# Optimization experiments

Measured on AMD Instinct MI355X. Metric: run time of the kernel, lower is better.

Reference implementation:

```python
import jax, jax.numpy as jnp
import numpy as np

B, S, D, E, H = 4, 2048, 1024, 8, 4096

def setup_inputs() -> dict:
    key = jax.random.key(0)
    ks = jax.random.split(key, 7)
    scale_d = 1.0 / np.sqrt(D)
    scale_h = 1.0 / np.sqrt(H)
    return {
        "x": jax.random.normal(ks[0], (B, S, D), dtype=jnp.float32),
        "Wr": jax.random.uniform(ks[1], (D, E), jnp.float32, -scale_d, scale_d),
        "br": jnp.zeros((E,), jnp.float32),
        "W1": jax.random.uniform(ks[2], (E, D, H), jnp.float32, -scale_d, scale_d),
        "b1": jax.random.uniform(ks[3], (E, H), jnp.float32, -scale_d, scale_d),
        "W2": jax.random.uniform(ks[4], (E, H, D), jnp.float32, -scale_h, scale_h),
        "b2": jax.random.uniform(ks[5], (E, D), jnp.float32, -scale_h, scale_h),
    }

def reference(x, Wr, br, W1, b1, W2, b2):
    # Router: softmax then argmax (top-1). Note: original does NOT scale
    # expert output by the routing weight and never applies capacity drop.
    route_logits = jnp.einsum("bsd,de->bse", x, Wr) + br
    routing_weights = jax.nn.softmax(route_logits, axis=-1)
    selected_expert = jnp.argmax(routing_weights, axis=-1)  # [B, S] int

    num_experts = W1.shape[0]
    out = jnp.zeros_like(x)
    # Fixed small loop over experts (structurally distinct weight slices);
    # select-by-mask keeps shapes static under jit.
    for e in range(num_experts):
        h = jax.nn.gelu(jnp.einsum("bsd,dh->bsh", x, W1[e]) + b1[e], approximate=False)
        y = jnp.einsum("bsh,hd->bsd", h, W2[e]) + b2[e]
        out = jnp.where((selected_expert == e)[..., None], y, out)
    return out
```

## Files before the change

kernel.cpp:

```cpp
#include <hip/hip_runtime.h>
#include <math.h>

#define TOK   8192
#define DD    1024
#define EE    8
#define HH    4096
#define MAXROWS 10240
#define MAXMT 40

typedef unsigned short u16;
typedef unsigned int   u32;
typedef __bf16 bf16x8 __attribute__((ext_vector_type(8)));
typedef float  f32x4  __attribute__((ext_vector_type(4)));

__device__ __forceinline__ u16 f2bf(float f) {
  union { float f; u32 u; } v; v.f = f;
  u32 r = v.u + 0x7fffu + ((v.u >> 16) & 1u);
  return (u16)(r >> 16);
}

__device__ __forceinline__ void gload16(const void* g, void* l) {
  __builtin_amdgcn_global_load_lds(
      (const __attribute__((address_space(1))) void*)g,
      (__attribute__((address_space(3))) void*)l, 16, 0, 0);
}

__global__ void k_init(int* rowmap, int* counts, int* fill) {
  int i = blockIdx.x * 256 + threadIdx.x;
  if (i < MAXROWS) rowmap[i] = -1;
  if (blockIdx.x == 0 && threadIdx.x < EE) { counts[threadIdx.x] = 0; fill[threadIdx.x] = 0; }
}

__global__ __launch_bounds__(256)
void k_route(const float* __restrict__ x, const float* __restrict__ Wr,
             const float* __restrict__ br, int* __restrict__ eid,
             int* __restrict__ counts, u16* __restrict__ xb) {
  int t = blockIdx.x * 4 + (threadIdx.x >> 6);
  int lt = threadIdx.x & 63;
  const float4* xr = (const float4*)(x + (size_t)t * DD);
  u16* xbr = xb + (size_t)t * DD;
  const float4* wrp = (const float4*)Wr;
  float acc[EE];
  #pragma unroll
  for (int e = 0; e < EE; ++e) acc[e] = 0.f;
  #pragma unroll
  for (int i = 0; i < 4; ++i) {
    int d4 = lt + 64 * i;
    float4 v = xr[d4];
    u32 p0 = (u32)f2bf(v.x) | ((u32)f2bf(v.y) << 16);
    u32 p1 = (u32)f2bf(v.z) | ((u32)f2bf(v.w) << 16);
    ((uint2*)xbr)[d4] = make_uint2(p0, p1);
    float vv[4] = { v.x, v.y, v.z, v.w };
    #pragma unroll
    for (int dd = 0; dd < 4; ++dd) {
      float xv = vv[dd];
      float4 a = wrp[(size_t)(d4 * 4 + dd) * 2];
      float4 b = wrp[(size_t)(d4 * 4 + dd) * 2 + 1];
      acc[0] += xv * a.x; acc[1] += xv * a.y; acc[2] += xv * a.z; acc[3] += xv * a.w;
      acc[4] += xv * b.x; acc[5] += xv * b.y; acc[6] += xv * b.z; acc[7] += xv * b.w;
    }
  }
  #pragma unroll
  for (int e = 0; e < EE; ++e)
    #pragma unroll
    for (int off = 32; off > 0; off >>= 1) acc[e] += __shfl_down(acc[e], off);
  if (lt == 0) {
    float best = -1e30f; int be = 0;
    #pragma unroll
    for (int e = 0; e < EE; ++e) {
      float v = acc[e] + br[e];
      if (v > best) { best = v; be = e; }
    }
    eid[t] = be;
    atomicAdd(&counts[be], 1);
  }
}

__global__ void k_scan(const int* __restrict__ counts, int* __restrict__ poff) {
  if (threadIdx.x == 0) {
    int off = 0; poff[0] = 0;
    for (int e = 0; e < EE; ++e) { off += ((counts[e] + 255) >> 8) << 8; poff[e + 1] = off; }
  }
}

__global__ void k_fillmap(const int* __restrict__ eid, const int* __restrict__ poff,
                          int* __restrict__ fill, int* __restrict__ rowmap) {
  int t = blockIdx.x * 256 + threadIdx.x;
  if (t < TOK) {
    int e = eid[t];
    int pos = atomicAdd(&fill[e], 1);
    rowmap[poff[e] + pos] = t;
  }
}

__global__ __launch_bounds__(256)
void k_transpose(const float* __restrict__ W, u16* __restrict__ WT, int K, int N) {
  __shared__ float tile[64][33];
  const int e = blockIdx.z;
  const int n0 = blockIdx.x * 32, k0 = blockIdx.y * 64;
  const float* We = W + (size_t)e * K * N;
  u16* WTe = WT + (size_t)e * K * N;
  const int t = threadIdx.x;
  const int kk = t >> 3, nn = (t & 7) * 4;
  #pragma unroll
  for (int i = 0; i < 2; ++i) {
    const float4 v = *(const float4*)&We[(size_t)(k0 + kk + 32 * i) * N + n0 + nn];
    tile[kk + 32 * i][nn]     = v.x;
    tile[kk + 32 * i][nn + 1] = v.y;
    tile[kk + 32 * i][nn + 2] = v.z;
    tile[kk + 32 * i][nn + 3] = v.w;
  }
  __syncthreads();
  const int n = t >> 3, c = t & 7;
  u32 p[4];
  #pragma unroll
  for (int j = 0; j < 4; ++j) {
    u32 lo = f2bf(tile[c * 8 + 2 * j][n]);
    u32 hi = f2bf(tile[c * 8 + 2 * j + 1][n]);
    p[j] = lo | (hi << 16);
  }
  *(uint4*)&WTe[(size_t)(n0 + n) * K + k0 + c * 8] = make_uint4(p[0], p[1], p[2], p[3]);
}

template <int KDIM, int NDIM, bool G2>
__global__ __launch_bounds__(512, 2)
void k_gemm(const u16* __restrict__ Abase, const u16* __restrict__ WT,
            const float* __restrict__ bias, const int* __restrict__ poff,
            const int* __restrict__ rowmap, u16* __restrict__ hout,
            float* __restrict__ yout) {
  extern __shared__ char lds[];
  const int mt = blockIdx.y;
  const int mbase = mt * 256;
  if (mbase >= poff[EE]) return;
  int e = 0;
  #pragma unroll
  for (int q = 1; q < EE; ++q) e += (mbase >= poff[q]) ? 1 : 0;

  const int nbase = blockIdx.x * 256;
  const int tid = threadIdx.x;
  const int lt = tid & 63;
  const int wid = tid >> 6;
  const int wr = wid >> 2, wc = wid & 3;

  const int row0 = tid >> 2;
  const int cl = (tid & 3) ^ ((tid >> 3) & 3);
  int r0, r1;
  if (G2) { r0 = mbase + row0; r1 = r0 + 128; }
  else {
    r0 = rowmap[mbase + row0];       if (r0 < 0) r0 = 0;
    r1 = rowmap[mbase + 128 + row0]; if (r1 < 0) r1 = 0;
  }
  const u16* gA0 = Abase + (size_t)r0 * KDIM + cl * 8;
  const u16* gA1 = Abase + (size_t)r1 * KDIM + cl * 8;
  const u16* wte = WT + (size_t)e * NDIM * KDIM + (size_t)nbase * KDIM;
  const u16* gB0 = wte + (size_t)row0 * KDIM + cl * 8;
  const u16* gB1 = wte + (size_t)(128 + row0) * KDIM + cl * 8;

  char* dA = lds + tid * 16;
  char* dB = lds + 65536 + tid * 16;

#define STAGE(B, T) do {                               \
    const int ko = (T) * 32;                           \
    gload16(gA0 + ko, dA + (B) * 16384);               \
    gload16(gA1 + ko, dA + (B) * 16384 + 8192);        \
    gload16(gB0 + ko, dB + (B) * 16384);               \
    gload16(gB1 + ko, dB + (B) * 16384 + 8192);        \
  } while (0)

  const int cph = ((lt >> 4) ^ ((lt >> 1) & 3)) << 4;
  const char* pA = lds + (wr * 128 + (lt & 15)) * 64 + cph;
  const char* pB = lds + 65536 + (wc * 64 + (lt & 15)) * 64 + cph;

  f32x4 acc[8][4] = {};

#define GSTEP(T, B, WAITI, DOSTAGE) do {                                              \
    asm volatile("s_waitcnt vmcnt(" WAITI ")\n\ts_barrier" ::: "memory");             \
    if (DOSTAGE) STAGE(((B) + 3) & 3, (T) + 3);                                       \
    bf16x8 af[8], bg[4];                                                              \
    _Pragma("unroll")                                                                 \
    for (int m = 0; m < 8; ++m) af[m] = *(const bf16x8*)(pA + (B) * 16384 + m * 1024);\
    _Pragma("unroll")                                                                 \
    for (int n = 0; n < 4; ++n) bg[n] = *(const bf16x8*)(pB + (B) * 16384 + n * 1024);\
    __builtin_amdgcn_s_setprio(1);                                                    \
    _Pragma("unroll")                                                                 \
    for (int m = 0; m < 8; ++m)                                                       \
      _Pragma("unroll")                                                               \
      for (int n = 0; n < 4; ++n)                                                     \
        acc[m][n] = __builtin_amdgcn_mfma_f32_16x16x32_bf16(af[m], bg[n], acc[m][n], 0, 0, 0); \
    __builtin_amdgcn_s_setprio(0);                                                    \
  } while (0)

  STAGE(0, 0); STAGE(1, 1); STAGE(2, 2);
  const int KT = KDIM / 32;
  #pragma unroll 1
  for (int kt = 0; kt < KT - 4; kt += 4) {
    GSTEP(kt + 0, 0, "8", true);
    GSTEP(kt + 1, 1, "8", true);
    GSTEP(kt + 2, 2, "8", true);
    GSTEP(kt + 3, 3, "8", true);
  }
  GSTEP(KT - 4, 0, "8", true);
  GSTEP(KT - 3, 1, "8", false);
  GSTEP(KT - 2, 2, "4", false);
  GSTEP(KT - 1, 3, "0", false);
#undef GSTEP
#undef STAGE

  const int cl16 = lt & 15, rq = (lt >> 4) * 4;
  float bv[4];
  #pragma unroll
  for (int n = 0; n < 4; ++n)
    bv[n] = bias[(size_t)e * NDIM + nbase + wc * 64 + n * 16 + cl16];

  const int colb = nbase + wc * 64 + cl16;
  #pragma unroll
  for (int m = 0; m < 8; ++m) {
    const int rb = mbase + wr * 128 + m * 16 + rq;
    #pragma unroll
    for (int r = 0; r < 4; ++r) {
      const int grow = rb + r;
      if (G2) {
        const int tok = rowmap[grow];
        if (tok >= 0) {
          float* yp = yout + (size_t)tok * NDIM + colb;
          #pragma unroll
          for (int n = 0; n < 4; ++n) yp[n * 16] = acc[m][n][r] + bv[n];
        }
      } else {
        u16* hp = hout + (size_t)grow * NDIM + colb;
        #pragma unroll
        for (int n = 0; n < 4; ++n) {
          float v = acc[m][n][r] + bv[n];
          v = 0.5f * v * (1.0f + erff(v * 0.70710678118654752f));
          hp[n * 16] = f2bf(v);
        }
      }
    }
  }
}

extern "C" void kernel_launch(void* const* d_in, const int* in_sizes, int n_in,
                              void* d_out, int out_size, void* d_ws, size_t ws_size,
                              hipStream_t stream) {
  const float* x  = (const float*)d_in[0];
  const float* Wr = (const float*)d_in[1];
  const float* br = (const float*)d_in[2];
  const float* W1 = (const float*)d_in[3];
  const float* b1 = (const float*)d_in[4];
  const float* W2 = (const float*)d_in[5];
  const float* b2 = (const float*)d_in[6];
  float* out = (float*)d_out;

  char* ws = (char*)d_ws;
  int* eid    = (int*)(ws + 0);
  int* counts = (int*)(ws + 32768);
  int* fill   = (int*)(ws + 32832);
  int* poff   = (int*)(ws + 32896);
  int* rowmap = (int*)(ws + 33024);
  u16* xbf    = (u16*)(ws + 73984);
  u16* w1t    = (u16*)(ws + 16851200);
  u16* w2t    = (u16*)(ws + 83960064);
  u16* hbuf   = (u16*)(ws + 151068928);

  hipFuncSetAttribute((const void*)k_gemm<DD, HH, false>,
                      hipFuncAttributeMaxDynamicSharedMemorySize, 131072);
  hipFuncSetAttribute((const void*)k_gemm<HH, DD, true>,
                      hipFuncAttributeMaxDynamicSharedMemorySize, 131072);

  k_init<<<MAXROWS / 256, 256, 0, stream>>>(rowmap, counts, fill);
  k_route<<<TOK / 4, 256, 0, stream>>>(x, Wr, br, eid, counts, xbf);
  k_scan<<<1, 64, 0, stream>>>(counts, poff);
  k_fillmap<<<TOK / 256, 256, 0, stream>>>(eid, poff, fill, rowmap);
  k_transpose<<<dim3(HH / 32, DD / 64, EE), 256, 0, stream>>>(W1, w1t, DD, HH);
  k_transpose<<<dim3(DD / 32, HH / 64, EE), 256, 0, stream>>>(W2, w2t, HH, DD);
  k_gemm<DD, HH, false><<<dim3(HH / 256, MAXMT), 512, 131072, stream>>>(xbf, w1t, b1, poff, rowmap, hbuf, nullptr);
  k_gemm<HH, DD, true><<<dim3(DD / 256, MAXMT), 512, 131072, stream>>>(hbuf, w2t, b2, poff, rowmap, nullptr, out);
}
```

Measured before the change: 692.1 us.

## Restructure GEMM main loop into double-buffered 64-wide K tiles with four-phase interleave

Replaces the 4-deep ring of 32-wide K stages with a double-buffered scheme of 64-wide K tiles. Each tile is split into four phases, each covering one K half and one M half. Global loads for the next tile are issued in slices between LDS fragment reads and MFMA blocks. The goal is finer interleaving of memory traffic with compute and halving the A-fragment register footprint, in exchange for more barriers per K step and shallower prefetch depth.

```diff
diff --git a/kernel.cpp b/kernel.cpp
--- a/kernel.cpp
+++ b/kernel.cpp
@@ -156,55 +156,73 @@
   const u16* gB0 = wte + (size_t)row0 * KDIM + cl * 8;
   const u16* gB1 = wte + (size_t)(128 + row0) * KDIM + cl * 8;
 
-  char* dA = lds + tid * 16;
-  char* dB = lds + 65536 + tid * 16;
-
-#define STAGE(B, T) do {                               \
-    const int ko = (T) * 32;                           \
-    gload16(gA0 + ko, dA + (B) * 16384);               \
-    gload16(gA1 + ko, dA + (B) * 16384 + 8192);        \
-    gload16(gB0 + ko, dB + (B) * 16384);               \
-    gload16(gB1 + ko, dB + (B) * 16384 + 8192);        \
-  } while (0)
+  char* sA = lds + tid * 16;
+  char* sB = lds + 65536 + tid * 16;
 
   const int cph = ((lt >> 4) ^ ((lt >> 1) & 3)) << 4;
   const char* pA = lds + (wr * 128 + (lt & 15)) * 64 + cph;
   const char* pB = lds + 65536 + (wc * 64 + (lt & 15)) * 64 + cph;
 
   f32x4 acc[8][4] = {};
-
-#define GSTEP(T, B, WAITI, DOSTAGE) do {                                              \
-    asm volatile("s_waitcnt vmcnt(" WAITI ")\n\ts_barrier" ::: "memory");             \
-    if (DOSTAGE) STAGE(((B) + 3) & 3, (T) + 3);                                       \
-    bf16x8 af[8], bg[4];                                                              \
-    _Pragma("unroll")                                                                 \
-    for (int m = 0; m < 8; ++m) af[m] = *(const bf16x8*)(pA + (B) * 16384 + m * 1024);\
-    _Pragma("unroll")                                                                 \
-    for (int n = 0; n < 4; ++n) bg[n] = *(const bf16x8*)(pB + (B) * 16384 + n * 1024);\
-    __builtin_amdgcn_s_setprio(1);                                                    \
-    _Pragma("unroll")                                                                 \
-    for (int m = 0; m < 8; ++m)                                                       \
-      _Pragma("unroll")                                                               \
-      for (int n = 0; n < 4; ++n)                                                     \
-        acc[m][n] = __builtin_amdgcn_mfma_f32_16x16x32_bf16(af[m], bg[n], acc[m][n], 0, 0, 0); \
-    __builtin_amdgcn_s_setprio(0);                                                    \
+  bf16x8 af[4], bg[4];
+
+#define STG_A(nb, kh, TOFF) do { \
+    gload16(gA0 + (TOFF) * 64 + (kh) * 32, sA + (nb) * 32768 + (kh) * 16384); \
+    gload16(gA1 + (TOFF) * 64 + (kh) * 32, sA + (nb) * 32768 + (kh) * 16384 + 8192); } while (0)
+#define STG_B(nb, kh, TOFF) do { \
+    gload16(gB0 + (TOFF) * 64 + (kh) * 32, sB + (nb) * 32768 + (kh) * 16384); \
+    gload16(gB1 + (TOFF) * 64 + (kh) * 32, sB + (nb) * 32768 + (kh) * 16384 + 8192); } while (0)
+
+#define PHASE(b, kh, mh, LOADB, STAGECODE, WAITSTR) do { \
+    _Pragma("unroll") \
+    for (int m = 0; m < 4; ++m) \
+      af[m] = *(const bf16x8*)(pA + (b) * 32768 + (kh) * 16384 + (mh) * 4096 + m * 1024); \
+    if (LOADB) { \
+      _Pragma("unroll") \
+      for (int n = 0; n < 4; ++n) \
+        bg[n] = *(const bf16x8*)(pB + (b) * 32768 + (kh) * 16384 + n * 1024); \
+    } \
+    STAGECODE; \
+    asm volatile(WAITSTR "s_barrier" ::: "memory"); \
+    asm volatile("s_waitcnt lgkmcnt(0)" ::: "memory"); \
+    __builtin_amdgcn_s_setprio(1); \
+    _Pragma("unroll") \
+    for (int m = 0; m < 4; ++m) \
+      _Pragma("unroll") \
+      for (int n = 0; n < 4; ++n) \
+        acc[(mh) * 4 + m][n] = \
+            __builtin_amdgcn_mfma_f32_16x16x32_bf16(af[m], bg[n], acc[(mh) * 4 + m][n], 0, 0, 0); \
+    __builtin_amdgcn_s_setprio(0); \
+    asm volatile("s_barrier" ::: "memory"); \
   } while (0)
 
-  STAGE(0, 0); STAGE(1, 1); STAGE(2, 2);
-  const int KT = KDIM / 32;
+#define TILE(b, SA0, SB0, SA1, SB1, W1S, W3S) do { \
+    PHASE(b, 0, 0, true,  SA0, ""); \
+    PHASE(b, 0, 1, false, SB0, W1S); \
+    PHASE(b, 1, 0, true,  SA1, ""); \
+    PHASE(b, 1, 1, false, SB1, W3S); \
+  } while (0)
+
+  STG_A(0, 0, 0); STG_B(0, 0, 0); STG_A(0, 1, 0); STG_B(0, 1, 0);
+  asm volatile("s_waitcnt vmcnt(4)\n\ts_barrier" ::: "memory");
+
+  const int KT = KDIM / 64;
   #pragma unroll 1
-  for (int kt = 0; kt < KT - 4; kt += 4) {
-    GSTEP(kt + 0, 0, "8", true);
-    GSTEP(kt + 1, 1, "8", true);
-    GSTEP(kt + 2, 2, "8", true);
-    GSTEP(kt + 3, 3, "8", true);
-  }
-  GSTEP(KT - 4, 0, "8", true);
-  GSTEP(KT - 3, 1, "8", false);
-  GSTEP(KT - 2, 2, "4", false);
-  GSTEP(KT - 1, 3, "0", false);
-#undef GSTEP
-#undef STAGE
+  for (int t = 0; t < KT - 2; t += 2) {
+    TILE(0, STG_A(1, 0, 1), STG_B(1, 0, 1), STG_A(1, 1, 1), STG_B(1, 1, 1),
+         "s_waitcnt vmcnt(4)\n\t", "s_waitcnt vmcnt(4)\n\t");
+    TILE(1, STG_A(0, 0, 2), STG_B(0, 0, 2), STG_A(0, 1, 2), STG_B(0, 1, 2),
+         "s_waitcnt vmcnt(4)\n\t", "s_waitcnt vmcnt(4)\n\t");
+    gA0 += 128; gA1 += 128; gB0 += 128; gB1 += 128;
+  }
+  TILE(0, STG_A(1, 0, 1), STG_B(1, 0, 1), STG_A(1, 1, 1), STG_B(1, 1, 1),
+       "s_waitcnt vmcnt(4)\n\t", "s_waitcnt vmcnt(4)\n\t");
+  TILE(1, (void)0, (void)0, (void)0, (void)0,
+       "s_waitcnt vmcnt(0)\n\t", "");
+#undef TILE
+#undef PHASE
+#undef STG_A
+#undef STG_B
 
   const int cl16 = lt & 15, rq = (lt >> 4) * 4;
   float bv[4];
```

New measurement: 690.2 us. About the same (-0.3%).
